# Optimization experiments

Hardware: AMD Instinct MI355X
Metric: run time of the kernel (lower is better)

Reference implementation:

```python
import jax, jax.numpy as jnp
import numpy as np

N = 50000   # nodes
E = 400000  # edges per relation
R = 3       # relations
IN, HID, C, H = 128, 64, 40, 3  # in_feat, hidden_feat, n_classes, num_heads
NEG_SLOPE = 0.2  # DGL GATConv default leaky_relu slope


def setup_inputs() -> dict:
    key = jax.random.key(0)
    ks = jax.random.split(key, 12)
    feat = jax.random.normal(ks[0], (N, IN), jnp.float32)
    src = jax.random.randint(ks[1], (R, E), 0, N, dtype=jnp.int32)
    dst = jax.random.randint(ks[2], (R, E), 0, N, dtype=jnp.int32)

    def w(k, shape, fan):
        return jax.random.normal(k, shape, jnp.float32) / np.float32(np.sqrt(fan))

    # layer 1: in_feat -> hidden_feat, relu activation
    W1 = w(ks[3], (R, IN, H * HID), IN)
    al1 = w(ks[4], (R, H, HID), HID)
    ar1 = w(ks[5], (R, H, HID), HID)
    b1 = jnp.zeros((R, H * HID), jnp.float32)
    # layer 2: hidden_feat -> n_classes, no activation
    W2 = w(ks[6], (R, HID, H * C), HID)
    al2 = w(ks[7], (R, H, C), C)
    ar2 = w(ks[8], (R, H, C), C)
    b2 = jnp.zeros((R, H * C), jnp.float32)
    return dict(feat=feat, src=src, dst=dst, W1=W1, al1=al1, ar1=ar1, b1=b1,
                W2=W2, al2=al2, ar2=ar2, b2=b2)


def gat_hetero_layer(feat, src, dst, W, al, ar, b, apply_relu):
    """HeteroGraphConv(mean) over R relations, each a GATConv + head-mean."""
    n = feat.shape[0]

    def one_relation(src_r, dst_r, W_r, al_r, ar_r, b_r):
        n_heads, out = al_r.shape
        z = (feat @ W_r).reshape(n, n_heads, out)          # [N,H,out]
        el = jnp.sum(z * al_r, axis=-1)                    # [N,H]
        er = jnp.sum(z * ar_r, axis=-1)                    # [N,H]
        e = jax.nn.leaky_relu(el[src_r] + er[dst_r], NEG_SLOPE)  # [E,H]
        # edge softmax over incoming edges of each dst node
        m = jax.ops.segment_max(e, dst_r, num_segments=n)  # [N,H]
        a = jnp.exp(e - m[dst_r])                          # [E,H]
        s = jax.ops.segment_sum(a, dst_r, num_segments=n)  # [N,H]
        alpha = a / s[dst_r]                               # [E,H]
        msg = alpha[:, :, None] * z[src_r]                 # [E,H,out]
        rst = jax.ops.segment_sum(msg, dst_r, num_segments=n)  # [N,H,out]
        rst = rst + b_r.reshape(n_heads, out)
        if apply_relu:
            rst = jax.nn.relu(rst)
        return rst.mean(axis=1)                            # head mean -> [N,out]

    outs = jax.vmap(one_relation)(src, dst, W, al, ar, b)  # [R,N,out]
    return outs.mean(axis=0)                               # relation mean


def reference(feat, src, dst, W1, al1, ar1, b1, W2, al2, ar2, b2):
    h = gat_hetero_layer(feat, src, dst, W1, al1, ar1, b1, True)
    h = gat_hetero_layer(h, src, dst, W2, al2, ar2, b2, False)
    return h
```

## Files before the change

### kernel.cpp

```cpp
#include <hip/hip_runtime.h>

#define R_   3
#define N_   50000
#define E_   400000
#define IN_  128
#define HID_ 64
#define C_   40
#define H_   3
#define NEG_SLOPE 0.2f
#define LOG2E 1.4426950408889634f

#define SCAN_CHUNK 1024
#define NCH  49
#define NCH2 64

#define MPAD 50048
#define NRT  3128

typedef _Float16 half_t;
typedef _Float16 f16x8 __attribute__((ext_vector_type(8)));
typedef _Float16 f16x4 __attribute__((ext_vector_type(4)));
typedef float float4v __attribute__((ext_vector_type(4)));

template <int V> struct vecT;
template <> struct vecT<4> { typedef f16x4 type; };
template <> struct vecT<8> { typedef f16x8 type; };


template <int K, int NY>
__device__ inline void bprep_body(int idx, const float* __restrict__ W,
                                  half_t* __restrict__ Bf, int Nc) {
    constexpr int KB = K / 32;
    const int TOT = R_ * NY * KB * 4 * 64;
    if (idx >= TOT) return;
    int lane = idx & 63;
    int ct = (idx >> 6) & 3;
    int t = idx >> 8;
    int kb = t % KB; t /= KB;
    int y = t % NY;  int r = t / NY;
    int col = y * 64 + ct * 16 + (lane & 15);
    int k0 = kb * 32 + (lane >> 4) * 8;
    f16x8 h = {};
    if (col < Nc) {
        #pragma unroll
        for (int j = 0; j < 8; ++j)
            h[j] = (half_t)W[((size_t)r * K + k0 + j) * Nc + col];
    }
    ((f16x8*)Bf)[idx] = h;
}

__global__ void prep_kernel(const float* __restrict__ feat, half_t* __restrict__ At,
                            const float* __restrict__ W1, half_t* __restrict__ B1f,
                            const float* __restrict__ W2, half_t* __restrict__ B2f,
                            int* __restrict__ deg, half_t* __restrict__ h1T) {
    int b = blockIdx.x;
    if (b < 3128) {
        int idx = b * 256 + threadIdx.x;
        int lane = idx & 63;
        int kb = (idx >> 6) & 3;
        int rowtile = idx >> 8;
        int row = rowtile * 16 + (lane & 15);
        int k = kb * 32 + (lane >> 4) * 8;
        f16x8 h = {};
        if (row < N_) {
            const float* p = feat + (size_t)row * IN_ + k;
            float4 a = ((const float4*)p)[0];
            float4 c = ((const float4*)p)[1];
            h[0] = (half_t)a.x; h[1] = (half_t)a.y; h[2] = (half_t)a.z; h[3] = (half_t)a.w;
            h[4] = (half_t)c.x; h[5] = (half_t)c.y; h[6] = (half_t)c.z; h[7] = (half_t)c.w;
        }
        ((f16x8*)At)[idx] = h;
    } else if (b < 3164) {
        bprep_body<IN_, 3>((b - 3128) * 256 + threadIdx.x, W1, B1f, H_ * HID_);
    } else if (b < 3188) {
        bprep_body<HID_, 2>((b - 3164) * 256 + threadIdx.x, W2, B2f, H_ * C_);
    } else if (b < 3774) {
        int i = (b - 3188) * 256 + threadIdx.x;
        if (i < R_ * N_) deg[i] = 0;
    } else {
        int i = (b - 3774) * 256 + threadIdx.x;
        if (i < 3072) h1T[(size_t)3125 * 2 * 512 + i] = (half_t)0.f;
    }
}

__global__ void hist_kernel(const int* __restrict__ dst, int* __restrict__ deg) {
    const int T = (R_ * E_) / 4;
    int t = blockIdx.x * 256 + threadIdx.x;
    if (t >= T) return;
    #pragma unroll
    for (int j = 0; j < 4; ++j) {
        int idx = t + j * T;
        int r = idx / E_;
        atomicAdd(&deg[r * N_ + dst[idx]], 1);
    }
}

__global__ void scanA_kernel(const int* __restrict__ deg, int* __restrict__ bsum) {
    int r = blockIdx.y, ch = blockIdx.x, tid = threadIdx.x;
    int base = ch * SCAN_CHUNK + tid * 4;
    int s = 0;
    for (int j = 0; j < 4; ++j) {
        int i = base + j;
        if (i < N_) s += deg[r * N_ + i];
    }
    __shared__ int red[256];
    red[tid] = s; __syncthreads();
    for (int off = 128; off; off >>= 1) {
        if (tid < off) red[tid] += red[tid + off];
        __syncthreads();
    }
    if (tid == 0) bsum[r * NCH2 + ch] = red[0];
}

__global__ void scanC_kernel(const int* __restrict__ deg, const int* __restrict__ bsum,
                             int* __restrict__ rowptr, int* __restrict__ cursor) {
    int r = blockIdx.y, ch = blockIdx.x, tid = threadIdx.x;
    __shared__ int chbase_s;
    if (tid < 64) {
        int v = (tid < NCH) ? bsum[r * NCH2 + tid] : 0;
        int s = v;
        #pragma unroll
        for (int off = 1; off < 64; off <<= 1) {
            int t = __shfl_up(s, off);
            if (tid >= off) s += t;
        }
        if (tid == ch) chbase_s = s - v;
    }
    int base = ch * SCAN_CHUNK + tid * 4;
    int v[4]; int s = 0;
    for (int j = 0; j < 4; ++j) {
        int i = base + j;
        v[j] = (i < N_) ? deg[r * N_ + i] : 0;
        s += v[j];
    }
    __shared__ int buf[256];
    buf[tid] = s; __syncthreads();
    for (int off = 1; off < 256; off <<= 1) {
        int t2 = (tid >= off) ? buf[tid - off] : 0;
        __syncthreads();
        buf[tid] += t2;
        __syncthreads();
    }
    int excl = buf[tid] - s + chbase_s;
    int run = excl;
    for (int j = 0; j < 4; ++j) {
        int i = base + j;
        if (i < N_) {
            rowptr[r * (N_ + 1) + i] = run;
            cursor[r * N_ + i] = run;
            run += v[j];
        }
    }
    if (ch == 0 && tid == 0) rowptr[r * (N_ + 1) + N_] = E_;
}

__global__ void fill_kernel(const int* __restrict__ src, const int* __restrict__ dst,
                            int* __restrict__ cursor, int* __restrict__ csr_src) {
    const int T = (R_ * E_) / 4;
    int t = blockIdx.x * 256 + threadIdx.x;
    if (t >= T) return;
    int pos[4], s3[4], rr[4];
    #pragma unroll
    for (int j = 0; j < 4; ++j) {
        int idx = t + j * T;
        rr[j] = idx / E_;
        pos[j] = atomicAdd(&cursor[rr[j] * N_ + dst[idx]], 1);
        s3[j] = src[idx] * 3;
    }
    #pragma unroll
    for (int j = 0; j < 4; ++j)
        csr_src[(size_t)rr[j] * E_ + pos[j]] = s3[j];
}

template <int K, int NY, bool FUSE>
__global__ __launch_bounds__(256) void mfma_gemm3_kernel(
        const half_t* __restrict__ At, const half_t* __restrict__ Bf,
        half_t* __restrict__ Z, int Nc,
        const float* __restrict__ al, const float* __restrict__ ar,
        float* __restrict__ el, float* __restrict__ er) {
    constexpr int KB = K / 32;
    int r = blockIdx.z, y = blockIdx.y;
    int wave = threadIdx.x >> 6, lane = threadIdx.x & 63;
    int rowtile = blockIdx.x * 4 + wave;
    const f16x8* Ap = (const f16x8*)At + (size_t)rowtile * KB * 64 + lane;
    const f16x8* Bp = (const f16x8*)Bf + (size_t)(r * NY + y) * KB * 4 * 64 + lane;
    float4v acc[4] = {};
    #pragma unroll
    for (int kb = 0; kb < KB; ++kb) {
        f16x8 af = Ap[kb * 64];
        #pragma unroll
        for (int ct = 0; ct < 4; ++ct) {
            f16x8 bf = Bp[(kb * 4 + ct) * 64];
            acc[ct] = __builtin_amdgcn_mfma_f32_16x16x32_f16(af, bf, acc[ct], 0, 0, 0);
        }
    }
    int lrow = lane & 15, lq = lane >> 4;
    half_t* Zr = Z + (size_t)r * N_ * Nc;
    int rbase = rowtile * 16 + lq * 4;
    int col0 = y * 64;
    float elv[4] = {}, erv[4] = {};
    const float* alp;
    const float* arp;
    if constexpr (FUSE) {
        alp = al + ((size_t)r * H_ + y) * 64;
        arp = ar + ((size_t)r * H_ + y) * 64;
    }
    #pragma unroll
    for (int ct = 0; ct < 4; ++ct) {
        int col = col0 + ct * 16 + lrow;
        if (col >= Nc) continue;
        float wa = 0.f, wb = 0.f;
        if constexpr (FUSE) { wa = alp[ct * 16 + lrow]; wb = arp[ct * 16 + lrow]; }
        #pragma unroll
        for (int g = 0; g < 4; ++g) {
            int row = rbase + g;
            half_t zh = (half_t)acc[ct][g];
            if (row < N_) Zr[(size_t)row * Nc + col] = zh;
            if constexpr (FUSE) {
                float zf = (float)zh;
                elv[g] = fmaf(zf, wa, elv[g]);
                erv[g] = fmaf(zf, wb, erv[g]);
            }
        }
    }
    if constexpr (FUSE) {
        #pragma unroll
        for (int g = 0; g < 4; ++g) {
            #pragma unroll
            for (int m = 1; m < 16; m <<= 1) {
                elv[g] += __shfl_xor(elv[g], m);
                erv[g] += __shfl_xor(erv[g], m);
            }
        }
        if (lrow == 0) {
            #pragma unroll
            for (int g = 0; g < 4; ++g) {
                int row = rbase + g;
                if (row < N_) {
                    size_t o = ((size_t)r * N_ + row) * H_ + y;
                    el[o] = elv[g] * LOG2E;
                    er[o] = erv[g] * LOG2E;
                }
            }
        }
    }
}

template <int Dd>
__global__ __launch_bounds__(256) void attn2_kernel(
        const half_t* __restrict__ z, const float* __restrict__ al,
        const float* __restrict__ ar, float* __restrict__ el,
        float* __restrict__ er) {
    int t = blockIdx.x * 256 + threadIdx.x;
    if (t >= R_ * N_ * H_) return;
    int rn = t / H_, h = t - rn * H_;
    int r = rn / N_;
    const half_t* zrow = z + (size_t)rn * (3 * Dd) + h * Dd;
    const float* alp = al + (r * H_ + h) * Dd;
    const float* arp = ar + (r * H_ + h) * Dd;
    float p0 = 0.f, p1 = 0.f, q0 = 0.f, q1 = 0.f;
    #pragma unroll
    for (int c = 0; c < Dd / 8; ++c) {
        f16x8 zv = *(const f16x8*)(zrow + c * 8);
        #pragma unroll
        for (int j = 0; j < 8; j += 2) {
            float za = (float)zv[j], zb = (float)zv[j + 1];
            p0 += za * alp[c * 8 + j];
            p1 += zb * alp[c * 8 + j + 1];
            q0 += za * arp[c * 8 + j];
            q1 += zb * arp[c * 8 + j + 1];
        }
    }
    el[t] = (p0 + p1) * LOG2E;
    er[t] = (q0 + q1) * LOG2E;
}

template <int Dd, int VEC, bool RELU, typename OutT, bool TILED>
__global__ __launch_bounds__(256) void agg15_kernel(
        const int* __restrict__ rowptr, const int* __restrict__ csr_src,
        const half_t* __restrict__ z, const float* __restrict__ el,
        const float* __restrict__ er, const float* __restrict__ bias,
        OutT* __restrict__ out, float scale) {
    constexpr int ROWH = 3 * Dd;
    constexpr int LPE  = ROWH / VEC;
    constexpr int PH   = Dd / VEC;
    using fv = typename vecT<VEC>::type;
    int n = blockIdx.x * 4 + (threadIdx.x >> 6);
    int lane = threadIdx.x & 63;
    if (n >= N_) return;
    int hf = lane >> 5;
    int sub = lane & 31;
    bool act = sub < LPE;
    int hl = act ? sub / PH : 0;
    int dl = act ? sub - hl * PH : 0;
    int zoff = VEC * sub;
    int ii[R_], ee[R_];
    float ervv[R_];
    #pragma unroll
    for (int r = 0; r < R_; ++r) {
        ii[r] = rowptr[r * (N_ + 1) + n];
        ee[r] = rowptr[r * (N_ + 1) + n + 1];
        ervv[r] = er[((size_t)r * N_ + n) * H_ + hl];
    }
    fv ah[R_] = {};
    float ll[R_] = {};
    bool any = (ii[0] < ee[0]) | (ii[1] < ee[1]) | (ii[2] < ee[2]);
    if (any) {
        int sA_c[R_], sB_c[R_], sA_n[R_], sB_n[R_];
        fv zA_c[R_], zB_c[R_];
        float eA_c[R_], eB_c[R_];
        #pragma unroll
        for (int r = 0; r < R_; ++r) {
            const int* cs = csr_src + (size_t)r * E_;
            int eA = ii[r] + hf, eB = ii[r] + 2 + hf;
            sA_c[r] = cs[eA < ee[r] ? eA : 0];
            sB_c[r] = cs[eB < ee[r] ? eB : 0];
        }
        #pragma unroll
        for (int r = 0; r < R_; ++r) {
            const half_t* zr = z + (size_t)r * N_ * ROWH;
            const float* elr = el + (size_t)r * N_ * H_;
            eA_c[r] = elr[sA_c[r] + hl];
            eB_c[r] = elr[sB_c[r] + hl];
            zA_c[r] = {}; zB_c[r] = {};
            if (act) {
                zA_c[r] = *(const fv*)(zr + (size_t)sA_c[r] * Dd + zoff);
                zB_c[r] = *(const fv*)(zr + (size_t)sB_c[r] * Dd + zoff);
            }
        }
        #pragma unroll
        for (int r = 0; r < R_; ++r) {
            const int* cs = csr_src + (size_t)r * E_;
            int eA = ii[r] + 4 + hf, eB = ii[r] + 6 + hf;
            sA_n[r] = cs[eA < ee[r] ? eA : 0];
            sB_n[r] = cs[eB < ee[r] ? eB : 0];
        }
        while (true) {
            fv zA_n[R_], zB_n[R_];
            float eA_n[R_], eB_n[R_];
            #pragma unroll
            for (int r = 0; r < R_; ++r) {
                const half_t* zr = z + (size_t)r * N_ * ROWH;
                const float* elr = el + (size_t)r * N_ * H_;
                eA_n[r] = elr[sA_n[r] + hl];
                eB_n[r] = elr[sB_n[r] + hl];
                zA_n[r] = {}; zB_n[r] = {};
                if (act) {
                    zA_n[r] = *(const fv*)(zr + (size_t)sA_n[r] * Dd + zoff);
                    zB_n[r] = *(const fv*)(zr + (size_t)sB_n[r] * Dd + zoff);
                }
            }
            int sA_2[R_], sB_2[R_];
            #pragma unroll
            for (int r = 0; r < R_; ++r) {
                const int* cs = csr_src + (size_t)r * E_;
                int eA = ii[r] + 8 + hf, eB = ii[r] + 10 + hf;
                sA_2[r] = cs[eA < ee[r] ? eA : 0];
                sB_2[r] = cs[eB < ee[r] ? eB : 0];
            }
            #pragma unroll
            for (int r = 0; r < R_; ++r) {
                int eA = ii[r] + hf, eB = ii[r] + 2 + hf;
                bool okA = eA < ee[r], okB = eB < ee[r];
                float xa = eA_c[r] + ervv[r]; xa = fmaxf(xa, NEG_SLOPE * xa);
                float xb = eB_c[r] + ervv[r]; xb = fmaxf(xb, NEG_SLOPE * xb);
                float cA = okA ? __builtin_amdgcn_exp2f(xa) : 0.f;
                float cB = okB ? __builtin_amdgcn_exp2f(xb) : 0.f;
                ll[r] += cA + cB;
                half_t hA = (half_t)cA, hB = (half_t)cB;
                fv vA, vB;
                #pragma unroll
                for (int v = 0; v < VEC; ++v) { vA[v] = hA; vB[v] = hB; }
                ah[r] += vA * zA_c[r] + vB * zB_c[r];
            }
            #pragma unroll
            for (int r = 0; r < R_; ++r) ii[r] += 4;
            if (!((ii[0] < ee[0]) | (ii[1] < ee[1]) | (ii[2] < ee[2]))) break;
            #pragma unroll
            for (int r = 0; r < R_; ++r) {
                sA_c[r] = sA_n[r]; sB_c[r] = sB_n[r];
                sA_n[r] = sA_2[r]; sB_n[r] = sB_2[r];
                zA_c[r] = zA_n[r]; zB_c[r] = zB_n[r];
                eA_c[r] = eA_n[r]; eB_c[r] = eB_n[r];
            }
        }
    }
    float aa[R_][VEC];
    #pragma unroll
    for (int r = 0; r < R_; ++r)
        #pragma unroll
        for (int v = 0; v < VEC; ++v) aa[r][v] = (float)ah[r][v];
    #pragma unroll
    for (int r = 0; r < R_; ++r) {
        #pragma unroll
        for (int v = 0; v < VEC; ++v) aa[r][v] += __shfl(aa[r][v], lane ^ 32);
        ll[r] += __shfl(ll[r], lane ^ 32);
    }
    float vacc[VEC] = {};
    #pragma unroll
    for (int r = 0; r < R_; ++r) {
        float li = (ll[r] > 0.f) ? 1.f / ll[r] : 0.f;
        const float* br = bias + r * ROWH + hl * Dd + VEC * dl;
        #pragma unroll
        for (int v = 0; v < VEC; ++v) {
            float t = aa[r][v] * li + br[v];
            if (RELU) t = fmaxf(t, 0.f);
            vacc[v] += t;
        }
    }
    int base = lane & 32;
    int p1 = sub + PH;     if (p1 >= LPE) p1 -= LPE;
    int p2 = sub + 2 * PH; if (p2 >= LPE) p2 -= LPE;
    #pragma unroll
    for (int v = 0; v < VEC; ++v)
        vacc[v] += __shfl(vacc[v], base + p1) + __shfl(vacc[v], base + p2);
    int srcl = lane / VEC;
    int cm = lane & (VEC - 1);
    float tv[VEC];
    #pragma unroll
    for (int v = 0; v < VEC; ++v) tv[v] = __shfl(vacc[v], srcl);
    float outv = tv[0];
    #pragma unroll
    for (int v = 1; v < VEC; ++v) outv = (cm == v) ? tv[v] : outv;
    if constexpr (TILED) {
        int rowtile = n >> 4;
        int kb = lane >> 5;
        int fl = (n & 15) + ((lane >> 3) & 3) * 16;
        int elo = lane & 7;
        size_t ho = (((size_t)rowtile * 2 + kb) * 64 + fl) * 8 + elo;
        ((half_t*)out)[ho] = (half_t)(outv * scale);
    } else {
        if (lane < Dd) out[(size_t)n * Dd + lane] = (OutT)(outv * scale);
    }
}

static inline size_t align256(size_t x) { return (x + 255) & ~(size_t)255; }

extern "C" void kernel_launch(void* const* d_in, const int* in_sizes, int n_in,
                              void* d_out, int out_size, void* d_ws, size_t ws_size,
                              hipStream_t stream) {
    const float* feat = (const float*)d_in[0];
    const int*   src  = (const int*)d_in[1];
    const int*   dst  = (const int*)d_in[2];
    const float* W1   = (const float*)d_in[3];
    const float* al1  = (const float*)d_in[4];
    const float* ar1  = (const float*)d_in[5];
    const float* b1   = (const float*)d_in[6];
    const float* W2   = (const float*)d_in[7];
    const float* al2  = (const float*)d_in[8];
    const float* ar2  = (const float*)d_in[9];
    const float* b2   = (const float*)d_in[10];
    float* out = (float*)d_out;

    char* ws = (char*)d_ws;
    size_t off = 0;
    half_t* zbuf  = (half_t*)(ws + off); off += align256((size_t)R_ * N_ * (3 * HID_) * 2);
    half_t* featT = (half_t*)(ws + off); off += align256((size_t)NRT * 4 * 64 * 8 * 2);
    half_t* h1T   = (half_t*)(ws + off); off += align256((size_t)NRT * 2 * 64 * 8 * 2);
    half_t* B1f   = (half_t*)(ws + off); off += align256((size_t)R_ * 3 * 4 * 4 * 64 * 8 * 2);
    half_t* B2f   = (half_t*)(ws + off); off += align256((size_t)R_ * 2 * 2 * 4 * 64 * 8 * 2);
    float* el   = (float*)(ws + off); off += align256((size_t)R_ * N_ * H_ * 4);
    float* er   = (float*)(ws + off); off += align256((size_t)R_ * N_ * H_ * 4);
    int* deg    = (int*)(ws + off);   off += align256((size_t)R_ * N_ * 4);
    int* rowptr = (int*)(ws + off);   off += align256((size_t)R_ * (N_ + 1) * 4);
    int* cursor = (int*)(ws + off);   off += align256((size_t)R_ * N_ * 4);
    int* bsum   = (int*)(ws + off);   off += align256((size_t)R_ * NCH2 * 4);
    int* csr    = (int*)(ws + off);   off += align256((size_t)R_ * E_ * 4);
    (void)ws_size; (void)n_in; (void)in_sizes; (void)out_size;

    const int ROW_TILES = (N_ + 63) / 64;
    const int NODE_WAVES = (N_ + 3) / 4;
    const int ATTN_BLOCKS = (R_ * N_ * H_ + 255) / 256;
    const int E4_BLOCKS = (R_ * E_ / 4 + 255) / 256;

    prep_kernel<<<3786, 256, 0, stream>>>(feat, featT, W1, B1f, W2, B2f, deg, h1T);

    hist_kernel<<<E4_BLOCKS, 256, 0, stream>>>(dst, deg);
    scanA_kernel<<<dim3(NCH, R_), 256, 0, stream>>>(deg, bsum);
    scanC_kernel<<<dim3(NCH, R_), 256, 0, stream>>>(deg, bsum, rowptr, cursor);
    fill_kernel<<<E4_BLOCKS, 256, 0, stream>>>(src, dst, cursor, csr);

    mfma_gemm3_kernel<IN_, 3, true><<<dim3(ROW_TILES, 3, R_), 256, 0, stream>>>(
        featT, B1f, zbuf, H_ * HID_, al1, ar1, el, er);
    agg15_kernel<HID_, 8, true, half_t, true><<<NODE_WAVES, 256, 0, stream>>>(
        rowptr, csr, zbuf, el, er, b1, h1T, 1.f / (H_ * R_));

    mfma_gemm3_kernel<HID_, 2, false><<<dim3(ROW_TILES, 2, R_), 256, 0, stream>>>(
        h1T, B2f, zbuf, H_ * C_, nullptr, nullptr, nullptr, nullptr);
    attn2_kernel<C_><<<ATTN_BLOCKS, 256, 0, stream>>>(zbuf, al2, ar2, el, er);
    agg15_kernel<C_, 4, false, float, false><<<NODE_WAVES, 256, 0, stream>>>(
        rowptr, csr, zbuf, el, er, b2, out, 1.f / (H_ * R_));
}
```

Before: 463.8 us.

## Precompute per-edge attention weights in separate kernel and simplify aggregation loop

Adds an alpha_kernel that computes unnormalized exp2 attention weights per CSR edge, using a new csr_dst3 array built during fill, and stores them as float4 per edge. The aggregation kernel now reads these weights instead of gathering el/er and computing leaky-relu and exp inline. Its software-pipelined prefetch loop is replaced by a plain loop. This moves the random el gather out of the aggregation critical path. In exchange it adds an extra kernel launch per layer, an extra edge-array write and read of about 19MB each, and loses the prefetch pipelining. Out-of-range reads are padded via extra zeroed csr entries.

Measured after the change: 473.3 us. 2.0% more time.

```diff
diff --git a/kernel.cpp b/kernel.cpp
--- a/kernel.cpp
+++ b/kernel.cpp
@@ -52,7 +52,8 @@
 __global__ void prep_kernel(const float* __restrict__ feat, half_t* __restrict__ At,
                             const float* __restrict__ W1, half_t* __restrict__ B1f,
                             const float* __restrict__ W2, half_t* __restrict__ B2f,
-                            int* __restrict__ deg, half_t* __restrict__ h1T) {
+                            int* __restrict__ deg, half_t* __restrict__ h1T,
+                            int* __restrict__ csr_src) {
     int b = blockIdx.x;
     if (b < 3128) {
         int idx = b * 256 + threadIdx.x;
@@ -77,9 +78,11 @@
     } else if (b < 3774) {
         int i = (b - 3188) * 256 + threadIdx.x;
         if (i < R_ * N_) deg[i] = 0;
-    } else {
+    } else if (b < 3786) {
         int i = (b - 3774) * 256 + threadIdx.x;
         if (i < 3072) h1T[(size_t)3125 * 2 * 512 + i] = (half_t)0.f;
+    } else {
+        if (threadIdx.x < 16) csr_src[(size_t)R_ * E_ + threadIdx.x] = 0;
     }
 }
 
@@ -155,21 +158,26 @@
 }
 
 __global__ void fill_kernel(const int* __restrict__ src, const int* __restrict__ dst,
-                            int* __restrict__ cursor, int* __restrict__ csr_src) {
+                            int* __restrict__ cursor, int* __restrict__ csr_src,
+                            int* __restrict__ csr_dst3) {
     const int T = (R_ * E_) / 4;
     int t = blockIdx.x * 256 + threadIdx.x;
     if (t >= T) return;
-    int pos[4], s3[4], rr[4];
+    int pos[4], s3[4], d3[4], rr[4];
     #pragma unroll
     for (int j = 0; j < 4; ++j) {
         int idx = t + j * T;
         rr[j] = idx / E_;
-        pos[j] = atomicAdd(&cursor[rr[j] * N_ + dst[idx]], 1);
+        int d = dst[idx];
+        pos[j] = atomicAdd(&cursor[rr[j] * N_ + d], 1);
         s3[j] = src[idx] * 3;
-    }
-    #pragma unroll
-    for (int j = 0; j < 4; ++j)
+        d3[j] = d * 3;
+    }
+    #pragma unroll
+    for (int j = 0; j < 4; ++j) {
         csr_src[(size_t)rr[j] * E_ + pos[j]] = s3[j];
+        csr_dst3[(size_t)rr[j] * E_ + pos[j]] = d3[j];
+    }
 }
 
 template <int K, int NY, bool FUSE>
@@ -275,12 +283,35 @@
     er[t] = (q0 + q1) * LOG2E;
 }
 
+__global__ __launch_bounds__(256) void alpha_kernel(
+        const int* __restrict__ csr_src, const int* __restrict__ csr_dst3,
+        const float* __restrict__ el, const float* __restrict__ er,
+        float* __restrict__ alpha) {
+    int r = blockIdx.y;
+    int p = blockIdx.x * 256 + threadIdx.x;
+    if (p >= E_) return;
+    size_t gp = (size_t)r * E_ + p;
+    int s3 = csr_src[gp];
+    int n3 = csr_dst3[gp];
+    const float* elr = el + (size_t)r * N_ * H_;
+    const float* err = er + (size_t)r * N_ * H_;
+    float4 o;
+    float a[3];
+    #pragma unroll
+    for (int h = 0; h < 3; ++h) {
+        float x = elr[s3 + h] + err[n3 + h];
+        x = fmaxf(x, NEG_SLOPE * x);
+        a[h] = __builtin_amdgcn_exp2f(x);
+    }
+    o.x = a[0]; o.y = a[1]; o.z = a[2]; o.w = 0.f;
+    ((float4*)alpha)[gp] = o;
+}
+
 template <int Dd, int VEC, bool RELU, typename OutT, bool TILED>
-__global__ __launch_bounds__(256) void agg15_kernel(
+__global__ __launch_bounds__(256) void agg16_kernel(
         const int* __restrict__ rowptr, const int* __restrict__ csr_src,
-        const half_t* __restrict__ z, const float* __restrict__ el,
-        const float* __restrict__ er, const float* __restrict__ bias,
-        OutT* __restrict__ out, float scale) {
+        const float* __restrict__ alpha, const half_t* __restrict__ z,
+        const float* __restrict__ bias, OutT* __restrict__ out, float scale) {
     constexpr int ROWH = 3 * Dd;
     constexpr int LPE  = ROWH / VEC;
     constexpr int PH   = Dd / VEC;
@@ -295,95 +326,46 @@
     int dl = act ? sub - hl * PH : 0;
     int zoff = VEC * sub;
     int ii[R_], ee[R_];
-    float ervv[R_];
     #pragma unroll
     for (int r = 0; r < R_; ++r) {
         ii[r] = rowptr[r * (N_ + 1) + n];
         ee[r] = rowptr[r * (N_ + 1) + n + 1];
-        ervv[r] = er[((size_t)r * N_ + n) * H_ + hl];
     }
     fv ah[R_] = {};
     float ll[R_] = {};
-    bool any = (ii[0] < ee[0]) | (ii[1] < ee[1]) | (ii[2] < ee[2]);
-    if (any) {
-        int sA_c[R_], sB_c[R_], sA_n[R_], sB_n[R_];
-        fv zA_c[R_], zB_c[R_];
-        float eA_c[R_], eB_c[R_];
+    while (ii[0] < ee[0] || ii[1] < ee[1] || ii[2] < ee[2]) {
+        fv zA[R_], zB[R_];
+        float aA[R_], aB[R_];
         #pragma unroll
         for (int r = 0; r < R_; ++r) {
             const int* cs = csr_src + (size_t)r * E_;
+            const float* al4 = alpha + (size_t)r * E_ * 4;
+            const half_t* zr = z + (size_t)r * N_ * ROWH;
             int eA = ii[r] + hf, eB = ii[r] + 2 + hf;
-            sA_c[r] = cs[eA < ee[r] ? eA : 0];
-            sB_c[r] = cs[eB < ee[r] ? eB : 0];
+            bool okA = eA < ee[r], okB = eB < ee[r];
+            int sA = cs[eA];
+            int sB = cs[eB];
+            float a0 = al4[(size_t)eA * 4 + hl];
+            float b0 = al4[(size_t)eB * 4 + hl];
+            aA[r] = okA ? a0 : 0.f;
+            aB[r] = okB ? b0 : 0.f;
+            zA[r] = {}; zB[r] = {};
+            if (act) {
+                zA[r] = *(const fv*)(zr + (size_t)sA * Dd + zoff);
+                zB[r] = *(const fv*)(zr + (size_t)sB * Dd + zoff);
+            }
         }
         #pragma unroll
         for (int r = 0; r < R_; ++r) {
-            const half_t* zr = z + (size_t)r * N_ * ROWH;
-            const float* elr = el + (size_t)r * N_ * H_;
-            eA_c[r] = elr[sA_c[r] + hl];
-            eB_c[r] = elr[sB_c[r] + hl];
-            zA_c[r] = {}; zB_c[r] = {};
-            if (act) {
-                zA_c[r] = *(const fv*)(zr + (size_t)sA_c[r] * Dd + zoff);
-                zB_c[r] = *(const fv*)(zr + (size_t)sB_c[r] * Dd + zoff);
-            }
-        }
-        #pragma unroll
-        for (int r = 0; r < R_; ++r) {
-            const int* cs = csr_src + (size_t)r * E_;
-            int eA = ii[r] + 4 + hf, eB = ii[r] + 6 + hf;
-            sA_n[r] = cs[eA < ee[r] ? eA : 0];
-            sB_n[r] = cs[eB < ee[r] ? eB : 0];
-        }
-        while (true) {
-            fv zA_n[R_], zB_n[R_];
-            float eA_n[R_], eB_n[R_];
+            ll[r] += aA[r] + aB[r];
+            half_t hA = (half_t)aA[r], hB = (half_t)aB[r];
+            fv vA, vB;
             #pragma unroll
-            for (int r = 0; r < R_; ++r) {
-                const half_t* zr = z + (size_t)r * N_ * ROWH;
-                const float* elr = el + (size_t)r * N_ * H_;
-                eA_n[r] = elr[sA_n[r] + hl];
-                eB_n[r] = elr[sB_n[r] + hl];
-                zA_n[r] = {}; zB_n[r] = {};
-                if (act) {
-                    zA_n[r] = *(const fv*)(zr + (size_t)sA_n[r] * Dd + zoff);
-                    zB_n[r] = *(const fv*)(zr + (size_t)sB_n[r] * Dd + zoff);
-                }
-            }
-            int sA_2[R_], sB_2[R_];
-            #pragma unroll
-            for (int r = 0; r < R_; ++r) {
-                const int* cs = csr_src + (size_t)r * E_;
-                int eA = ii[r] + 8 + hf, eB = ii[r] + 10 + hf;
-                sA_2[r] = cs[eA < ee[r] ? eA : 0];
-                sB_2[r] = cs[eB < ee[r] ? eB : 0];
-            }
-            #pragma unroll
-            for (int r = 0; r < R_; ++r) {
-                int eA = ii[r] + hf, eB = ii[r] + 2 + hf;
-                bool okA = eA < ee[r], okB = eB < ee[r];
-                float xa = eA_c[r] + ervv[r]; xa = fmaxf(xa, NEG_SLOPE * xa);
-                float xb = eB_c[r] + ervv[r]; xb = fmaxf(xb, NEG_SLOPE * xb);
-                float cA = okA ? __builtin_amdgcn_exp2f(xa) : 0.f;
-                float cB = okB ? __builtin_amdgcn_exp2f(xb) : 0.f;
-                ll[r] += cA + cB;
-                half_t hA = (half_t)cA, hB = (half_t)cB;
-                fv vA, vB;
-                #pragma unroll
-                for (int v = 0; v < VEC; ++v) { vA[v] = hA; vB[v] = hB; }
-                ah[r] += vA * zA_c[r] + vB * zB_c[r];
-            }
-            #pragma unroll
-            for (int r = 0; r < R_; ++r) ii[r] += 4;
-            if (!((ii[0] < ee[0]) | (ii[1] < ee[1]) | (ii[2] < ee[2]))) break;
-            #pragma unroll
-            for (int r = 0; r < R_; ++r) {
-                sA_c[r] = sA_n[r]; sB_c[r] = sB_n[r];
-                sA_n[r] = sA_2[r]; sB_n[r] = sB_2[r];
-                zA_c[r] = zA_n[r]; zB_c[r] = zB_n[r];
-                eA_c[r] = eA_n[r]; eB_c[r] = eB_n[r];
-            }
-        }
+            for (int v = 0; v < VEC; ++v) { vA[v] = hA; vB[v] = hB; }
+            ah[r] += vA * zA[r] + vB * zB[r];
+        }
+        #pragma unroll
+        for (int r = 0; r < R_; ++r) ii[r] += 4;
     }
     float aa[R_][VEC];
     #pragma unroll
@@ -465,29 +447,34 @@
     int* rowptr = (int*)(ws + off);   off += align256((size_t)R_ * (N_ + 1) * 4);
     int* cursor = (int*)(ws + off);   off += align256((size_t)R_ * N_ * 4);
     int* bsum   = (int*)(ws + off);   off += align256((size_t)R_ * NCH2 * 4);
-    int* csr    = (int*)(ws + off);   off += align256((size_t)R_ * E_ * 4);
+    int* csr    = (int*)(ws + off);   off += align256((size_t)R_ * E_ * 4 + 64);
+    int* csrd3  = (int*)(ws + off);   off += align256((size_t)R_ * E_ * 4);
+    float* alphaB = (float*)(ws + off); off += align256(((size_t)R_ * E_ * 4 + 64) * 4);
     (void)ws_size; (void)n_in; (void)in_sizes; (void)out_size;
 
     const int ROW_TILES = (N_ + 63) / 64;
     const int NODE_WAVES = (N_ + 3) / 4;
     const int ATTN_BLOCKS = (R_ * N_ * H_ + 255) / 256;
     const int E4_BLOCKS = (R_ * E_ / 4 + 255) / 256;
-
-    prep_kernel<<<3786, 256, 0, stream>>>(feat, featT, W1, B1f, W2, B2f, deg, h1T);
+    const int ALPHA_BLOCKS = (E_ + 255) / 256;
+
+    prep_kernel<<<3787, 256, 0, stream>>>(feat, featT, W1, B1f, W2, B2f, deg, h1T, csr);
 
     hist_kernel<<<E4_BLOCKS, 256, 0, stream>>>(dst, deg);
     scanA_kernel<<<dim3(NCH, R_), 256, 0, stream>>>(deg, bsum);
     scanC_kernel<<<dim3(NCH, R_), 256, 0, stream>>>(deg, bsum, rowptr, cursor);
-    fill_kernel<<<E4_BLOCKS, 256, 0, stream>>>(src, dst, cursor, csr);
+    fill_kernel<<<E4_BLOCKS, 256, 0, stream>>>(src, dst, cursor, csr, csrd3);
 
     mfma_gemm3_kernel<IN_, 3, true><<<dim3(ROW_TILES, 3, R_), 256, 0, stream>>>(
         featT, B1f, zbuf, H_ * HID_, al1, ar1, el, er);
-    agg15_kernel<HID_, 8, true, half_t, true><<<NODE_WAVES, 256, 0, stream>>>(
-        rowptr, csr, zbuf, el, er, b1, h1T, 1.f / (H_ * R_));
+    alpha_kernel<<<dim3(ALPHA_BLOCKS, R_), 256, 0, stream>>>(csr, csrd3, el, er, alphaB);
+    agg16_kernel<HID_, 8, true, half_t, true><<<NODE_WAVES, 256, 0, stream>>>(
+        rowptr, csr, alphaB, zbuf, b1, h1T, 1.f / (H_ * R_));
 
     mfma_gemm3_kernel<HID_, 2, false><<<dim3(ROW_TILES, 2, R_), 256, 0, stream>>>(
         h1T, B2f, zbuf, H_ * C_, nullptr, nullptr, nullptr, nullptr);
     attn2_kernel<C_><<<ATTN_BLOCKS, 256, 0, stream>>>(zbuf, al2, ar2, el, er);
-    agg15_kernel<C_, 4, false, float, false><<<NODE_WAVES, 256, 0, stream>>>(
-        rowptr, csr, zbuf, el, er, b2, out, 1.f / (H_ * R_));
-}
+    alpha_kernel<<<dim3(ALPHA_BLOCKS, R_), 256, 0, stream>>>(csr, csrd3, el, er, alphaB);
+    agg16_kernel<C_, 4, false, float, false><<<NODE_WAVES, 256, 0, stream>>>(
+        rowptr, csr, alphaB, zbuf, b2, out, 1.f / (H_ * R_));
+}
```
